# Kernel tuning notes

Hardware: AMD Instinct MI355X
Metric: run time of the kernel (lower is better)

The kernel has to match this reference:

```python
import jax, jax.numpy as jnp
import numpy as np

B, S, D, H, E, F = 2, 1024, 1024, 16, 8, 4096
HD = D // H
EPS = 1e-5


def setup_inputs() -> dict:
    key = jax.random.key(0)
    ks = jax.random.split(key, 16)
    sc = 0.02
    return {
        "src": jax.random.normal(ks[0], (B, S, D), jnp.float32),
        "in_proj_w": jax.random.normal(ks[1], (3 * D, D), jnp.float32) * sc,
        "in_proj_b": jnp.zeros((3 * D,), jnp.float32),
        "out_w": jax.random.normal(ks[2], (D, D), jnp.float32) * sc,
        "out_b": jnp.zeros((D,), jnp.float32),
        "gate_w": jax.random.normal(ks[3], (E, D), jnp.float32) * sc,
        "gate_b": jnp.zeros((E,), jnp.float32),
        "w1": jax.random.normal(ks[4], (E, F, D), jnp.float32) * sc,
        "b1": jnp.zeros((E, F), jnp.float32),
        "w2": jax.random.normal(ks[5], (E, D, F), jnp.float32) * sc,
        "b2": jnp.zeros((E, D), jnp.float32),
        "ln1_g": jnp.ones((D,), jnp.float32),
        "ln1_b": jnp.zeros((D,), jnp.float32),
        "ln2_g": jnp.ones((D,), jnp.float32),
        "ln2_b": jnp.zeros((D,), jnp.float32),
    }


def layer_norm(x, g, b):
    mu = jnp.mean(x, axis=-1, keepdims=True)
    var = jnp.mean(jnp.square(x - mu), axis=-1, keepdims=True)
    return (x - mu) * jax.lax.rsqrt(var + EPS) * g + b


def mha(x, in_proj_w, in_proj_b, out_w, out_b):
    # torch nn.MultiheadAttention, batch_first, self-attention, eval mode
    qkv = x @ in_proj_w.T + in_proj_b  # (B,S,3D)
    q, k, v = jnp.split(qkv, 3, axis=-1)
    q = q.reshape(B, S, H, HD).transpose(0, 2, 1, 3)  # bhsd
    k = k.reshape(B, S, H, HD).transpose(0, 2, 1, 3)
    v = v.reshape(B, S, H, HD).transpose(0, 2, 1, 3)
    scores = jnp.einsum("bhqd,bhkd->bhqk", q, k) / np.sqrt(HD).astype(np.float32)
    attn = jax.nn.softmax(scores, axis=-1)
    o = jnp.einsum("bhqk,bhkd->bhqd", attn, v)
    o = o.transpose(0, 2, 1, 3).reshape(B, S, D)
    return o @ out_w.T + out_b


def moe(x, gate_w, gate_b, w1, b1, w2, b2, top_k=2):
    gate_logits = x @ gate_w.T + gate_b  # (B,S,E)
    topk_logits, topk_idx = jax.lax.top_k(gate_logits, top_k)
    topk_probs = jax.nn.softmax(topk_logits, axis=-1)  # (B,S,K)
    # dense per-expert weight: prob if in top-k else 0
    onehot = jax.nn.one_hot(topk_idx, E, dtype=x.dtype)  # (B,S,K,E)
    w_dense = jnp.einsum("bske,bsk->bse", onehot, topk_probs)
    # faithful to original: all experts computed densely, then mask-weighted
    h = jnp.einsum("bsd,efd->besf", x, w1) + b1[None, :, None, :]
    h = jax.nn.gelu(h, approximate=False)
    eo = jnp.einsum("besf,edf->besd", h, w2) + b2[None, :, None, :]
    out = jnp.einsum("besd,bse->bsd", eo, w_dense)
    usage = jnp.mean(jax.nn.softmax(gate_logits, axis=-1), axis=(0, 1))
    aux_loss = E * jnp.sum(usage ** 2)
    return out, aux_loss


def reference(src, in_proj_w, in_proj_b, out_w, out_b, gate_w, gate_b,
              w1, b1, w2, b2, ln1_g, ln1_b, ln2_g, ln2_b):
    attn_out = mha(src, in_proj_w, in_proj_b, out_w, out_b)
    x = layer_norm(src + attn_out, ln1_g, ln1_b)
    moe_out, aux_loss = moe(x, gate_w, gate_b, w1, b1, w2, b2)
    x = layer_norm(x + moe_out, ln2_g, ln2_b)
    return x, aux_loss
```

## Files before the change

kernel.cpp:

```cpp
#include <hip/hip_runtime.h>
#include <stdint.h>
#include <stddef.h>

#define T_TOK 2048
#define DMODEL 1024
#define NHEAD 16
#define HDIM 64
#define NEXP 8
#define FDIM 4096
#define SLEN 1024
#define NBATCH 2
#define LN_EPS 1e-5f

typedef unsigned short u16;
typedef __attribute__((ext_vector_type(8))) short s16x8;
typedef __attribute__((ext_vector_type(4))) float f32x4;
typedef __attribute__((ext_vector_type(4))) unsigned short u16x4;
typedef __attribute__((ext_vector_type(8))) unsigned short u16x8;

typedef __attribute__((address_space(1))) void gvoid;
typedef __attribute__((address_space(3))) void lvoid;

__device__ __forceinline__ u16 f2bf(float x) {
  union { float f; unsigned int u; } v; v.f = x;
  unsigned int r = v.u + 0x7fffu + ((v.u >> 16) & 1u);
  return (u16)(r >> 16);
}

__device__ __forceinline__ void gl_lds16(const u16* g, u16* lds_base) {
  __builtin_amdgcn_global_load_lds((gvoid*)g, (lvoid*)lds_base, 16, 0, 0);
}

__device__ __forceinline__ void cvt_body(const float* __restrict__ x,
                                         u16* __restrict__ y, long n4) {
  long i = (long)blockIdx.x * 256 + threadIdx.x;
  if (i >= n4) return;
  float4 v = ((const float4*)x)[i];
  u16x4 o;
  o[0] = f2bf(v.x); o[1] = f2bf(v.y); o[2] = f2bf(v.z); o[3] = f2bf(v.w);
  ((u16x4*)y)[i] = o;
}
__global__ __launch_bounds__(256) void cvt_small(const float* x, u16* y, long n4) { cvt_body(x, y, n4); }
__global__ __launch_bounds__(256) void cvt_w1(const float* x, u16* y, long n4) { cvt_body(x, y, n4); }
__global__ __launch_bounds__(256) void cvt_w2(const float* x, u16* y, long n4) { cvt_body(x, y, n4); }

template<int BM, int OUTBF, int DOGELU>
__device__ __forceinline__ void gemm_body(
    const u16* __restrict__ A, long lda,
    const u16* __restrict__ Bp, long ldb,
    char* __restrict__ C, long ldc,
    const float* __restrict__ bias,
    int Mloc, int k0start, int Kc, int m0, int n0) {
  constexpr int AS_BYTES = 2 * BM * 64 * 2;
  constexpr int SMEM_BYTES = AS_BYTES + 2 * 128 * 64 * 2;
  __shared__ __align__(16) char smem[SMEM_BYTES];
  u16 (*As)[BM][64]  = reinterpret_cast<u16(*)[BM][64]>(smem);
  u16 (*Bs)[128][64] = reinterpret_cast<u16(*)[128][64]>(smem + AS_BYTES);

  constexpr int SM = BM / 32;
  constexpr int LPI = BM / 32 + 4;

  int tid = threadIdx.x;
  int lane = tid & 63, w = tid >> 6;
  int lrow = lane >> 3;
  int sg8 = ((lane & 7) ^ lrow) * 8;
  int q = lane >> 4, rr = lane & 15;
  int wm = (w & 1) * (BM / 2), wn = (w >> 1) * 64;
  int NIT = Kc >> 6;

  auto issue = [&](int kt, int b) {
    int k0 = k0start + (kt << 6);
    for (int p = 0; p < BM / 32; p++) {
      int rb = p * 32 + w * 8;
      int gr = m0 + rb + lrow; if (gr > Mloc - 1) gr = Mloc - 1;
      gl_lds16(A + (long)gr * lda + k0 + sg8, &As[b][rb][0]);
    }
    for (int p = 0; p < 4; p++) {
      int rb = p * 32 + w * 8;
      gl_lds16(Bp + (long)(n0 + rb + lrow) * ldb + k0 + sg8, &Bs[b][rb][0]);
    }
  };

  f32x4 acc[SM][4];
  for (int i = 0; i < SM; i++)
    for (int j = 0; j < 4; j++)
      for (int r = 0; r < 4; r++) acc[i][j][r] = 0.f;

  issue(0, 0);
  if (NIT > 1) issue(1, 1);

  int slot0 = ((q ^ (rr & 7)) * 8);
  int slot1 = (((4 + q) ^ (rr & 7)) * 8);

  for (int kt = 0; kt < NIT; kt++) {
    int b = kt & 1;
    if (kt + 1 < NIT)
      asm volatile("s_waitcnt vmcnt(%0)" :: "i"(LPI) : "memory");
    else
      asm volatile("s_waitcnt vmcnt(0)" ::: "memory");
    asm volatile("s_barrier" ::: "memory");

    s16x8 a0[SM], a1[SM], b0[4], b1[4];
    for (int i = 0; i < SM; i++) {
      a0[i] = *(const s16x8*)&As[b][wm + i * 16 + rr][slot0];
      a1[i] = *(const s16x8*)&As[b][wm + i * 16 + rr][slot1];
    }
    for (int j = 0; j < 4; j++) {
      b0[j] = *(const s16x8*)&Bs[b][wn + j * 16 + rr][slot0];
      b1[j] = *(const s16x8*)&Bs[b][wn + j * 16 + rr][slot1];
    }
    asm volatile("s_waitcnt lgkmcnt(0)" ::: "memory");
    asm volatile("s_barrier" ::: "memory");
    if (kt + 2 < NIT) issue(kt + 2, b);

    for (int i = 0; i < SM; i++)
      for (int j = 0; j < 4; j++) {
        acc[i][j] = __builtin_amdgcn_mfma_f32_16x16x32_bf16(a0[i], b0[j], acc[i][j], 0, 0, 0);
        acc[i][j] = __builtin_amdgcn_mfma_f32_16x16x32_bf16(a1[i], b1[j], acc[i][j], 0, 0, 0);
      }
  }

  u16*   Cu = (u16*)smem;
  float* Cf = (float*)smem;
  for (int i = 0; i < SM; i++)
    for (int j = 0; j < 4; j++) {
      int col = wn + j * 16 + rr;
      float bv = bias ? bias[n0 + col] : 0.f;
      for (int r = 0; r < 4; r++) {
        int row = wm + i * 16 + q * 4 + r;
        float v = acc[i][j][r] + bv;
        if (DOGELU) v = 0.5f * v * (1.f + erff(v * 0.70710678118f));
        if (OUTBF) Cu[row * 128 + col] = f2bf(v);
        else       Cf[row * 128 + col] = v;
      }
    }
  __syncthreads();
  if (OUTBF) {
    for (int p = 0; p < BM / 16; p++) {
      int row = p * 16 + (tid >> 4);
      int co  = (tid & 15) * 8;
      if (m0 + row < Mloc) {
        u16x8 vv = *(const u16x8*)&Cu[row * 128 + co];
        *(u16x8*)((u16*)C + (long)(m0 + row) * ldc + n0 + co) = vv;
      }
    }
  } else {
    for (int p = 0; p < BM / 8; p++) {
      int row = p * 8 + (tid >> 5);
      int co  = (tid & 31) * 4;
      if (m0 + row < Mloc) {
        float4 vv = *(const float4*)&Cf[row * 128 + co];
        *(float4*)((float*)C + (long)(m0 + row) * ldc + n0 + co) = vv;
      }
    }
  }
}

__global__ __launch_bounds__(256) void k_qkv(const u16* __restrict__ A,
                                             const u16* __restrict__ B,
                                             u16* __restrict__ C,
                                             const float* __restrict__ bias) {
  gemm_body<64, 1, 0>(A, DMODEL, B, DMODEL, (char*)C, 3 * DMODEL, bias,
                      T_TOK, 0, DMODEL, blockIdx.y * 64, blockIdx.x * 128);
}

__global__ __launch_bounds__(256) void k_outp(const u16* __restrict__ A,
                                              const u16* __restrict__ B,
                                              float* __restrict__ Cpart) {
  int z = blockIdx.z;
  char* C = (char*)(Cpart + (long)z * T_TOK * DMODEL);
  gemm_body<64, 0, 0>(A, DMODEL, B, DMODEL, C, DMODEL, nullptr,
                      T_TOK, z * 512, 512, blockIdx.y * 64, blockIdx.x * 128);
}

__global__ __launch_bounds__(256) void k_ffn1(const u16* __restrict__ Ag,
                                              const u16* __restrict__ Bg,
                                              u16* __restrict__ Cg,
                                              const float* __restrict__ biasg,
                                              const int* __restrict__ cntp,
                                              const int* __restrict__ offp) {
  int z = blockIdx.z;
  int Mloc = cntp[z];
  int m0 = blockIdx.y * 128;
  if (m0 >= Mloc) return;
  long o = offp[z];
  gemm_body<128, 1, 1>(Ag + o * DMODEL, DMODEL,
                       Bg + (long)z * FDIM * DMODEL, DMODEL,
                       (char*)(Cg + o * FDIM), FDIM,
                       biasg + (long)z * FDIM,
                       Mloc, 0, DMODEL, m0, blockIdx.x * 128);
}

__global__ __launch_bounds__(256) void k_ffn2(const u16* __restrict__ Ag,
                                              const u16* __restrict__ Bg,
                                              float* __restrict__ Cpart,
                                              const int* __restrict__ cntp,
                                              const int* __restrict__ offp) {
  int zz = blockIdx.z;
  int z = zz & 7, kh = zz >> 3;
  int Mloc = cntp[z];
  int m0 = blockIdx.y * 128;
  if (m0 >= Mloc) return;
  long o = offp[z];
  float* C = Cpart + (long)kh * 2 * T_TOK * DMODEL;
  gemm_body<128, 0, 0>(Ag + o * FDIM, FDIM,
                       Bg + (long)z * DMODEL * FDIM, FDIM,
                       (char*)(C + o * DMODEL), DMODEL,
                       nullptr,
                       Mloc, kh * 2048, 2048, m0, blockIdx.x * 128);
}

__global__ __launch_bounds__(256) void transpose_v(const u16* __restrict__ qkv,
                                                   u16* __restrict__ vt) {
  __shared__ u16 tile[64][65];
  int s0 = blockIdx.x * 64, bh = blockIdx.y;
  int b = bh >> 4, h = bh & 15;
  int r = threadIdx.x >> 3, c = (threadIdx.x & 7) * 8;
  for (int p = 0; p < 64; p += 32) {
    u16x8 v = *(const u16x8*)&qkv[(long)(b * SLEN + s0 + p + r) * 3072 + 2048 + h * 64 + c];
    for (int j = 0; j < 8; j++) tile[p + r][c + j] = v[j];
  }
  __syncthreads();
  for (int p = 0; p < 64; p += 32) {
    int d = p + r;
    u16x8 v;
    for (int j = 0; j < 8; j++) v[j] = tile[c + j][d];
    *(u16x8*)&vt[((long)bh * 64 + d) * SLEN + s0 + c] = v;
  }
}

__global__ __launch_bounds__(256) void fused_attn(const u16* __restrict__ qkv,
                                                  const u16* __restrict__ vt,
                                                  u16* __restrict__ o2) {
  __shared__ u16 Qs[128][64];
  __shared__ u16 Ks[2][64][64];
  __shared__ u16 Vs[2][64][64];
  __shared__ u16 Ps[128][72];

  int qt = blockIdx.x, bh = blockIdx.y;
  int b = bh >> 4, h = bh & 15;
  const u16* base = qkv + (long)b * SLEN * 3072 + h * 64;
  const u16* vbase = vt + (long)bh * HDIM * SLEN;

  int tid = threadIdx.x, lane = tid & 63, w = tid >> 6;
  int lrow = lane >> 3;
  int sg8 = ((lane & 7) ^ lrow) * 8;
  int q = lane >> 4, rr = lane & 15;
  int wm = w * 32;

  auto issue_kv = [&](int kt, int bf) {
    for (int p = 0; p < 2; p++) {
      int rb = p * 32 + w * 8;
      gl_lds16(base + (long)(kt * 64 + rb + lrow) * 3072 + 1024 + sg8, &Ks[bf][rb][0]);
      gl_lds16(vbase + (long)(rb + lrow) * SLEN + kt * 64 + sg8, &Vs[bf][rb][0]);
    }
  };

  for (int p = 0; p < 4; p++) {
    int rb = p * 32 + w * 8;
    gl_lds16(base + (long)(qt * 128 + rb + lrow) * 3072 + sg8, &Qs[rb][0]);
  }
  issue_kv(0, 0);

  f32x4 O[2][4];
  float mi[2][4], li[2][4];
  for (int i = 0; i < 2; i++)
    for (int r = 0; r < 4; r++) { mi[i][r] = -1e30f; li[i][r] = 0.f; }
  for (int i = 0; i < 2; i++)
    for (int jn = 0; jn < 4; jn++)
      for (int r = 0; r < 4; r++) O[i][jn][r] = 0.f;

  for (int kt = 0; kt < 16; kt++) {
    int bf = kt & 1;
    asm volatile("s_waitcnt vmcnt(0)" ::: "memory");
    asm volatile("s_barrier" ::: "memory");
    if (kt + 1 < 16) issue_kv(kt + 1, bf ^ 1);

    f32x4 S[2][4];
    for (int i = 0; i < 2; i++)
      for (int j = 0; j < 4; j++)
        for (int r = 0; r < 4; r++) S[i][j][r] = 0.f;
    for (int ks = 0; ks < 2; ks++) {
      int slot = (((ks * 4 + q) ^ (rr & 7)) * 8);
      s16x8 aq0 = *(const s16x8*)&Qs[wm + rr][slot];
      s16x8 aq1 = *(const s16x8*)&Qs[wm + 16 + rr][slot];
      for (int j = 0; j < 4; j++) {
        s16x8 bk = *(const s16x8*)&Ks[bf][j * 16 + rr][slot];
        S[0][j] = __builtin_amdgcn_mfma_f32_16x16x32_bf16(aq0, bk, S[0][j], 0, 0, 0);
        S[1][j] = __builtin_amdgcn_mfma_f32_16x16x32_bf16(aq1, bk, S[1][j], 0, 0, 0);
      }
    }

    for (int i = 0; i < 2; i++) {
      for (int r = 0; r < 4; r++) {
        float mx = -1e30f;
        for (int j = 0; j < 4; j++) mx = fmaxf(mx, S[i][j][r]);
        for (int o = 1; o < 16; o <<= 1) mx = fmaxf(mx, __shfl_xor(mx, o));
        mx *= 0.125f;
        float mnew = fmaxf(mi[i][r], mx);
        float al = __expf(mi[i][r] - mnew);
        mi[i][r] = mnew;
        float ps = 0.f;
        for (int j = 0; j < 4; j++) {
          float e = __expf(S[i][j][r] * 0.125f - mnew);
          S[i][j][r] = e;
          ps += e;
        }
        for (int o = 1; o < 16; o <<= 1) ps += __shfl_xor(ps, o);
        li[i][r] = li[i][r] * al + ps;
        for (int jn = 0; jn < 4; jn++) O[i][jn][r] *= al;
      }
    }

    for (int i = 0; i < 2; i++)
      for (int j = 0; j < 4; j++)
        for (int r = 0; r < 4; r++)
          Ps[wm + i * 16 + q * 4 + r][j * 16 + rr] = f2bf(S[i][j][r]);

    for (int ks = 0; ks < 2; ks++) {
      s16x8 ap0 = *(const s16x8*)&Ps[wm + rr][ks * 32 + q * 8];
      s16x8 ap1 = *(const s16x8*)&Ps[wm + 16 + rr][ks * 32 + q * 8];
      int slot = (((ks * 4 + q) ^ (rr & 7)) * 8);
      for (int jn = 0; jn < 4; jn++) {
        s16x8 bv = *(const s16x8*)&Vs[bf][jn * 16 + rr][slot];
        O[0][jn] = __builtin_amdgcn_mfma_f32_16x16x32_bf16(ap0, bv, O[0][jn], 0, 0, 0);
        O[1][jn] = __builtin_amdgcn_mfma_f32_16x16x32_bf16(ap1, bv, O[1][jn], 0, 0, 0);
      }
    }
  }

  __syncthreads();
  u16* Pf = &Ps[0][0];
  for (int i = 0; i < 2; i++)
    for (int r = 0; r < 4; r++) {
      float inv = 1.f / li[i][r];
      int row = wm + i * 16 + q * 4 + r;
      for (int jn = 0; jn < 4; jn++)
        Pf[row * 64 + jn * 16 + rr] = f2bf(O[i][jn][r] * inv);
    }
  __syncthreads();
  for (int p = 0; p < 4; p++) {
    int row = p * 32 + (tid >> 3);
    int co  = (tid & 7) * 8;
    u16x8 vv = *(const u16x8*)&Pf[row * 64 + co];
    int s = qt * 128 + row;
    *(u16x8*)&o2[((long)(b * SLEN + s)) * DMODEL + h * 64 + co] = vv;
  }
}

__global__ __launch_bounds__(256) void add_ln(const float* __restrict__ a,
                                              const float* __restrict__ p0,
                                              const float* __restrict__ p1,
                                              const float* __restrict__ ob,
                                              const float* __restrict__ g,
                                              const float* __restrict__ bb,
                                              float* __restrict__ xf, u16* __restrict__ xb) {
  int t = blockIdx.x, tid = threadIdx.x;
  float4 va = ((const float4*)(a + (long)t * DMODEL))[tid];
  float4 v0v = ((const float4*)(p0 + (long)t * DMODEL))[tid];
  float4 v1v = ((const float4*)(p1 + (long)t * DMODEL))[tid];
  float4 vo = ((const float4*)ob)[tid];
  float v0 = va.x + v0v.x + v1v.x + vo.x;
  float v1 = va.y + v0v.y + v1v.y + vo.y;
  float v2 = va.z + v0v.z + v1v.z + vo.z;
  float v3 = va.w + v0v.w + v1v.w + vo.w;
  float s = v0 + v1 + v2 + v3;
  float s2 = v0 * v0 + v1 * v1 + v2 * v2 + v3 * v3;
  __shared__ float sa[4], sb[4];
  for (int o = 32; o; o >>= 1) { s += __shfl_down(s, o); s2 += __shfl_down(s2, o); }
  int lane = tid & 63, w = tid >> 6;
  if (lane == 0) { sa[w] = s; sb[w] = s2; }
  __syncthreads();
  s = sa[0] + sa[1] + sa[2] + sa[3];
  s2 = sb[0] + sb[1] + sb[2] + sb[3];
  float mu = s * (1.f / DMODEL);
  float var = s2 * (1.f / DMODEL) - mu * mu;
  float rs = rsqrtf(var + LN_EPS);
  float4 gg = ((const float4*)g)[tid];
  float4 bv = ((const float4*)bb)[tid];
  float4 o;
  o.x = (v0 - mu) * rs * gg.x + bv.x;
  o.y = (v1 - mu) * rs * gg.y + bv.y;
  o.z = (v2 - mu) * rs * gg.z + bv.z;
  o.w = (v3 - mu) * rs * gg.w + bv.w;
  ((float4*)(xf + (long)t * DMODEL))[tid] = o;
  u16x4 obv;
  obv[0] = f2bf(o.x); obv[1] = f2bf(o.y); obv[2] = f2bf(o.z); obv[3] = f2bf(o.w);
  ((u16x4*)(xb + (long)t * DMODEL))[tid] = obv;
}

__global__ __launch_bounds__(256) void gate_kernel(
    const float* __restrict__ xf, const float* __restrict__ gw, const float* __restrict__ gb,
    int* __restrict__ cnt, int* __restrict__ tok_list,
    int* __restrict__ tk_e, int* __restrict__ tk_pos, float* __restrict__ tk_prob,
    float* __restrict__ usage) {
  int wid = threadIdx.x >> 6, lane = threadIdx.x & 63;
  int t = blockIdx.x * 4 + wid;
  float xv[16];
  for (int j = 0; j < 16; j++) xv[j] = xf[(long)t * DMODEL + j * 64 + lane];
  float l[8];
  for (int e = 0; e < 8; e++) {
    float d = 0.f;
    for (int j = 0; j < 16; j++) d += xv[j] * gw[e * DMODEL + j * 64 + lane];
    for (int o = 32; o; o >>= 1) d += __shfl_down(d, o);
    l[e] = d;
  }
  __shared__ float us[8];
  if (threadIdx.x < 8) us[threadIdx.x] = 0.f;
  __syncthreads();
  if (lane == 0) {
    float mx = -1e30f;
    for (int e = 0; e < 8; e++) { l[e] += gb[e]; mx = fmaxf(mx, l[e]); }
    float ex[8], sum = 0.f;
    for (int e = 0; e < 8; e++) { ex[e] = expf(l[e] - mx); sum += ex[e]; }
    float inv = 1.f / sum;
    for (int e = 0; e < 8; e++) atomicAdd(&us[e], ex[e] * inv);
    int i1 = 0;
    for (int e = 1; e < 8; e++) if (l[e] > l[i1]) i1 = e;
    int i2 = (i1 == 0) ? 1 : 0;
    for (int e = 0; e < 8; e++) if (e != i1 && l[e] > l[i2]) i2 = e;
    float bb = expf(l[i2] - l[i1]);
    float p1 = 1.f / (1.f + bb), p2 = bb / (1.f + bb);
    int pos1 = atomicAdd(&cnt[i1], 1);
    tok_list[i1 * 2048 + pos1] = t;
    tk_e[2 * t] = i1; tk_pos[2 * t] = pos1; tk_prob[2 * t] = p1;
    int pos2 = atomicAdd(&cnt[i2], 1);
    tok_list[i2 * 2048 + pos2] = t;
    tk_e[2 * t + 1] = i2; tk_pos[2 * t + 1] = pos2; tk_prob[2 * t + 1] = p2;
  }
  __syncthreads();
  if (threadIdx.x < 8) atomicAdd(&usage[threadIdx.x], us[threadIdx.x]);
}

__global__ void finalize_gate(const int* __restrict__ cnt, int* __restrict__ offp,
                              const float* __restrict__ usage, float* __restrict__ aux_out) {
  if (threadIdx.x == 0) {
    int o = 0;
    for (int e = 0; e < 8; e++) { offp[e] = o; o += cnt[e]; }
    float s = 0.f;
    for (int e = 0; e < 8; e++) { float u = usage[e] * (1.f / T_TOK); s += u * u; }
    aux_out[0] = (float)NEXP * s;
  }
}

__global__ __launch_bounds__(256) void gather_x(const u16* __restrict__ xb,
                                                const int* __restrict__ cnt,
                                                const int* __restrict__ offp,
                                                const int* __restrict__ tok_list,
                                                u16* __restrict__ xg) {
  int e = blockIdx.y, i = blockIdx.x;
  if (i >= cnt[e]) return;
  int t = tok_list[e * 2048 + i];
  long j = offp[e] + i;
  ((uint2*)(xg + j * DMODEL))[threadIdx.x] =
      ((const uint2*)(xb + (long)t * DMODEL))[threadIdx.x];
}

__global__ __launch_bounds__(256) void moe_ln2(
    const float* __restrict__ xf, const float* __restrict__ y,
    const float* __restrict__ b2g,
    const int* __restrict__ offp, const int* __restrict__ tk_e,
    const int* __restrict__ tk_pos, const float* __restrict__ tk_prob,
    const float* __restrict__ g, const float* __restrict__ bb, float* __restrict__ out) {
  const long HALF = (long)2 * T_TOK * DMODEL;
  int t = blockIdx.x, tid = threadIdx.x;
  int e0 = tk_e[2 * t], e1 = tk_e[2 * t + 1];
  long j0 = (long)offp[e0] + tk_pos[2 * t];
  long j1 = (long)offp[e1] + tk_pos[2 * t + 1];
  float p0 = tk_prob[2 * t], p1 = tk_prob[2 * t + 1];
  float4 vx = ((const float4*)(xf + (long)t * DMODEL))[tid];
  float4 y0a = ((const float4*)(y + j0 * DMODEL))[tid];
  float4 y0b = ((const float4*)(y + HALF + j0 * DMODEL))[tid];
  float4 y1a = ((const float4*)(y + j1 * DMODEL))[tid];
  float4 y1b = ((const float4*)(y + HALF + j1 * DMODEL))[tid];
  float4 b0v = ((const float4*)(b2g + (long)e0 * DMODEL))[tid];
  float4 b1v = ((const float4*)(b2g + (long)e1 * DMODEL))[tid];
  float v0 = vx.x + p0 * (y0a.x + y0b.x + b0v.x) + p1 * (y1a.x + y1b.x + b1v.x);
  float v1 = vx.y + p0 * (y0a.y + y0b.y + b0v.y) + p1 * (y1a.y + y1b.y + b1v.y);
  float v2 = vx.z + p0 * (y0a.z + y0b.z + b0v.z) + p1 * (y1a.z + y1b.z + b1v.z);
  float v3 = vx.w + p0 * (y0a.w + y0b.w + b0v.w) + p1 * (y1a.w + y1b.w + b1v.w);
  float s = v0 + v1 + v2 + v3;
  float s2 = v0 * v0 + v1 * v1 + v2 * v2 + v3 * v3;
  __shared__ float sa[4], sb[4];
  for (int o = 32; o; o >>= 1) { s += __shfl_down(s, o); s2 += __shfl_down(s2, o); }
  int lane = tid & 63, w = tid >> 6;
  if (lane == 0) { sa[w] = s; sb[w] = s2; }
  __syncthreads();
  s = sa[0] + sa[1] + sa[2] + sa[3];
  s2 = sb[0] + sb[1] + sb[2] + sb[3];
  float mu = s * (1.f / DMODEL);
  float var = s2 * (1.f / DMODEL) - mu * mu;
  float rs = rsqrtf(var + LN_EPS);
  float4 gg = ((const float4*)g)[tid];
  float4 bv = ((const float4*)bb)[tid];
  float4 o;
  o.x = (v0 - mu) * rs * gg.x + bv.x;
  o.y = (v1 - mu) * rs * gg.y + bv.y;
  o.z = (v2 - mu) * rs * gg.z + bv.z;
  o.w = (v3 - mu) * rs * gg.w + bv.w;
  ((float4*)(out + (long)t * DMODEL))[tid] = o;
}

extern "C" void kernel_launch(void* const* d_in, const int* in_sizes, int n_in,
                              void* d_out, int out_size, void* d_ws, size_t ws_size,
                              hipStream_t stream) {
  const float* src  = (const float*)d_in[0];
  const float* inw  = (const float*)d_in[1];
  const float* inb  = (const float*)d_in[2];
  const float* outw = (const float*)d_in[3];
  const float* outb = (const float*)d_in[4];
  const float* gw   = (const float*)d_in[5];
  const float* gb   = (const float*)d_in[6];
  const float* w1   = (const float*)d_in[7];
  const float* b1   = (const float*)d_in[8];
  const float* w2   = (const float*)d_in[9];
  const float* b2   = (const float*)d_in[10];
  const float* g1   = (const float*)d_in[11];
  const float* bb1  = (const float*)d_in[12];
  const float* g2   = (const float*)d_in[13];
  const float* bb2  = (const float*)d_in[14];
  float* out = (float*)d_out;

  char* w = (char*)d_ws;
  auto alloc = [&](size_t bytes) {
    char* p = w;
    w += (bytes + 255) & ~(size_t)255;
    return p;
  };

  int*   cnt     = (int*)alloc(8 * 4);
  int*   offp    = (int*)alloc(8 * 4);
  float* usage   = (float*)alloc(8 * 4);
  int*   tok_list= (int*)alloc((size_t)NEXP * 2048 * 4);
  int*   tk_e    = (int*)alloc((size_t)2 * T_TOK * 4);
  int*   tk_pos  = (int*)alloc((size_t)2 * T_TOK * 4);
  float* tk_prob = (float*)alloc((size_t)2 * T_TOK * 4);

  u16* src_bf  = (u16*)alloc((size_t)T_TOK * DMODEL * 2);
  u16* inw_bf  = (u16*)alloc((size_t)3 * DMODEL * DMODEL * 2);
  u16* outw_bf = (u16*)alloc((size_t)DMODEL * DMODEL * 2);
  u16* w1_bf   = (u16*)alloc((size_t)NEXP * FDIM * DMODEL * 2);
  u16* w2_bf   = (u16*)alloc((size_t)NEXP * DMODEL * FDIM * 2);
  u16* qkv_bf  = (u16*)alloc((size_t)T_TOK * 3 * DMODEL * 2);
  u16* vt_bf   = (u16*)alloc((size_t)T_TOK * DMODEL * 2);
  u16* o2_bf   = (u16*)alloc((size_t)T_TOK * DMODEL * 2);
  float* attn_p= (float*)alloc((size_t)2 * T_TOK * DMODEL * 4);
  float* x_f   = (float*)alloc((size_t)T_TOK * DMODEL * 4);
  u16* x_bf    = (u16*)alloc((size_t)T_TOK * DMODEL * 2);
  u16* xg_bf   = (u16*)alloc((size_t)2 * T_TOK * DMODEL * 2);
  u16* h_bf    = (u16*)alloc((size_t)2 * T_TOK * FDIM * 2);
  float* y_f   = (float*)alloc((size_t)4 * T_TOK * DMODEL * 4);
  (void)ws_size; (void)n_in; (void)in_sizes; (void)out_size;

  hipMemsetAsync(cnt, 0, 3 * 256, stream);

  cvt_small<<<(T_TOK * DMODEL / 4 + 255) / 256, 256, 0, stream>>>(src, src_bf, T_TOK * DMODEL / 4);
  cvt_small<<<(3 * DMODEL * DMODEL / 4 + 255) / 256, 256, 0, stream>>>(inw, inw_bf, 3L * DMODEL * DMODEL / 4);
  cvt_small<<<(DMODEL * DMODEL / 4 + 255) / 256, 256, 0, stream>>>(outw, outw_bf, (long)DMODEL * DMODEL / 4);
  cvt_w1<<<(int)((long)NEXP * FDIM * DMODEL / 4 / 256), 256, 0, stream>>>(w1, w1_bf, (long)NEXP * FDIM * DMODEL / 4);
  cvt_w2<<<(int)((long)NEXP * DMODEL * FDIM / 4 / 256), 256, 0, stream>>>(w2, w2_bf, (long)NEXP * DMODEL * FDIM / 4);

  k_qkv<<<dim3(24, 32), 256, 0, stream>>>(src_bf, inw_bf, qkv_bf, inb);

  transpose_v<<<dim3(16, 32), 256, 0, stream>>>(qkv_bf, vt_bf);

  fused_attn<<<dim3(8, 32), 256, 0, stream>>>(qkv_bf, vt_bf, o2_bf);

  k_outp<<<dim3(8, 32, 2), 256, 0, stream>>>(o2_bf, outw_bf, attn_p);

  add_ln<<<T_TOK, 256, 0, stream>>>(src, attn_p, attn_p + (long)T_TOK * DMODEL,
                                    outb, g1, bb1, x_f, x_bf);

  gate_kernel<<<T_TOK / 4, 256, 0, stream>>>(x_f, gw, gb, cnt, tok_list,
                                             tk_e, tk_pos, tk_prob, usage);
  finalize_gate<<<1, 64, 0, stream>>>(cnt, offp, usage, out + (long)T_TOK * DMODEL);

  gather_x<<<dim3(2048, 8), 256, 0, stream>>>(x_bf, cnt, offp, tok_list, xg_bf);

  k_ffn1<<<dim3(32, 16, 8), 256, 0, stream>>>(xg_bf, w1_bf, h_bf, b1, cnt, offp);

  k_ffn2<<<dim3(8, 16, 16), 256, 0, stream>>>(h_bf, w2_bf, y_f, cnt, offp);

  moe_ln2<<<T_TOK, 256, 0, stream>>>(x_f, y_f, b2, offp, tk_e, tk_pos, tk_prob,
                                     g2, bb2, out);
}
```

Measured before the change: 645.8 us.

## Precompute GEMM load pointers, use fast GELU approximation, enlarge QKV tile

The GEMM loader now computes its per-row global pointers once and advances them by a fixed stride each K step, instead of recomputing addresses on every issue. The exact erf-based GELU in the FFN1 epilogue is replaced by an exp-and-reciprocal sigmoid approximation, which is cheaper but differs slightly from exact GELU. The QKV projection switches from 64-row to 128-row tiles, halving the grid to 384 blocks. The larger tile improves operand reuse but gives fewer blocks to fill the GPU's compute units.

Measured after the change: 634.0 us. Within noise of the previous version (-1.8%).

```diff
diff --git a/kernel.cpp b/kernel.cpp
--- a/kernel.cpp
+++ b/kernel.cpp
@@ -29,6 +29,12 @@
 
 __device__ __forceinline__ void gl_lds16(const u16* g, u16* lds_base) {
   __builtin_amdgcn_global_load_lds((gvoid*)g, (lvoid*)lds_base, 16, 0, 0);
+}
+
+__device__ __forceinline__ float gelu_fast(float v) {
+  float vv = v * v;
+  float e = __expf(v * (-1.5957691216f - 0.0713548162f * vv));
+  return v * __builtin_amdgcn_rcpf(1.f + e);
 }
 
 __device__ __forceinline__ void cvt_body(const float* __restrict__ x,
@@ -58,7 +64,8 @@
   u16 (*Bs)[128][64] = reinterpret_cast<u16(*)[128][64]>(smem + AS_BYTES);
 
   constexpr int SM = BM / 32;
-  constexpr int LPI = BM / 32 + 4;
+  constexpr int NPA = BM / 32;
+  constexpr int LPI = NPA + 4;
 
   int tid = threadIdx.x;
   int lane = tid & 63, w = tid >> 6;
@@ -68,16 +75,28 @@
   int wm = (w & 1) * (BM / 2), wn = (w >> 1) * 64;
   int NIT = Kc >> 6;
 
-  auto issue = [&](int kt, int b) {
-    int k0 = k0start + (kt << 6);
-    for (int p = 0; p < BM / 32; p++) {
-      int rb = p * 32 + w * 8;
-      int gr = m0 + rb + lrow; if (gr > Mloc - 1) gr = Mloc - 1;
-      gl_lds16(A + (long)gr * lda + k0 + sg8, &As[b][rb][0]);
-    }
+  const u16* aP[NPA];
+  const u16* bP[4];
+#pragma unroll
+  for (int p = 0; p < NPA; p++) {
+    int gr = m0 + p * 32 + w * 8 + lrow;
+    if (gr > Mloc - 1) gr = Mloc - 1;
+    aP[p] = A + (long)gr * lda + k0start + sg8;
+  }
+#pragma unroll
+  for (int p = 0; p < 4; p++)
+    bP[p] = Bp + (long)(n0 + p * 32 + w * 8 + lrow) * ldb + k0start + sg8;
+
+  auto issue = [&](int b) {
+#pragma unroll
+    for (int p = 0; p < NPA; p++) {
+      gl_lds16(aP[p], &As[b][p * 32 + w * 8][0]);
+      aP[p] += 64;
+    }
+#pragma unroll
     for (int p = 0; p < 4; p++) {
-      int rb = p * 32 + w * 8;
-      gl_lds16(Bp + (long)(n0 + rb + lrow) * ldb + k0 + sg8, &Bs[b][rb][0]);
+      gl_lds16(bP[p], &Bs[b][p * 32 + w * 8][0]);
+      bP[p] += 64;
     }
   };
 
@@ -86,8 +105,8 @@
     for (int j = 0; j < 4; j++)
       for (int r = 0; r < 4; r++) acc[i][j][r] = 0.f;
 
-  issue(0, 0);
-  if (NIT > 1) issue(1, 1);
+  issue(0);
+  if (NIT > 1) issue(1);
 
   int slot0 = ((q ^ (rr & 7)) * 8);
   int slot1 = (((4 + q) ^ (rr & 7)) * 8);
@@ -111,7 +130,7 @@
     }
     asm volatile("s_waitcnt lgkmcnt(0)" ::: "memory");
     asm volatile("s_barrier" ::: "memory");
-    if (kt + 2 < NIT) issue(kt + 2, b);
+    if (kt + 2 < NIT) issue(b);
 
     for (int i = 0; i < SM; i++)
       for (int j = 0; j < 4; j++) {
@@ -129,7 +148,7 @@
       for (int r = 0; r < 4; r++) {
         int row = wm + i * 16 + q * 4 + r;
         float v = acc[i][j][r] + bv;
-        if (DOGELU) v = 0.5f * v * (1.f + erff(v * 0.70710678118f));
+        if (DOGELU) v = gelu_fast(v);
         if (OUTBF) Cu[row * 128 + col] = f2bf(v);
         else       Cf[row * 128 + col] = v;
       }
@@ -160,8 +179,8 @@
                                              const u16* __restrict__ B,
                                              u16* __restrict__ C,
                                              const float* __restrict__ bias) {
-  gemm_body<64, 1, 0>(A, DMODEL, B, DMODEL, (char*)C, 3 * DMODEL, bias,
-                      T_TOK, 0, DMODEL, blockIdx.y * 64, blockIdx.x * 128);
+  gemm_body<128, 1, 0>(A, DMODEL, B, DMODEL, (char*)C, 3 * DMODEL, bias,
+                       T_TOK, 0, DMODEL, blockIdx.y * 128, blockIdx.x * 128);
 }
 
 __global__ __launch_bounds__(256) void k_outp(const u16* __restrict__ A,
@@ -560,7 +579,7 @@
   cvt_w1<<<(int)((long)NEXP * FDIM * DMODEL / 4 / 256), 256, 0, stream>>>(w1, w1_bf, (long)NEXP * FDIM * DMODEL / 4);
   cvt_w2<<<(int)((long)NEXP * DMODEL * FDIM / 4 / 256), 256, 0, stream>>>(w2, w2_bf, (long)NEXP * DMODEL * FDIM / 4);
 
-  k_qkv<<<dim3(24, 32), 256, 0, stream>>>(src_bf, inw_bf, qkv_bf, inb);
+  k_qkv<<<dim3(24, 16), 256, 0, stream>>>(src_bf, inw_bf, qkv_bf, inb);
 
   transpose_v<<<dim3(16, 32), 256, 0, stream>>>(qkv_bf, vt_bf);
 
```
